# Optimization experiments

Measured on AMD Instinct MI355X. Metric: run time of the kernel, lower is better.

Reference implementation:

```python
import jax, jax.numpy as jnp
import numpy as np

N_EMBD = 1024
N_HEAD = 16
B, T = 4, 2048


def setup_inputs() -> dict:
    key = jax.random.key(0)
    k1, k2, k3, k4, k5 = jax.random.split(key, 5)
    s = 0.02
    return {
        "x": jax.random.normal(k1, (B, T, N_EMBD), dtype=jnp.float32),
        "w_attn": jax.random.normal(k2, (N_EMBD, 3 * N_EMBD), dtype=jnp.float32) * s,
        "b_attn": jnp.zeros((3 * N_EMBD,), dtype=jnp.float32),
        "w_proj": jax.random.normal(k3, (N_EMBD, N_EMBD), dtype=jnp.float32) * s,
        "b_proj": jnp.zeros((N_EMBD,), dtype=jnp.float32),
    }


def reference(x, w_attn, b_attn, w_proj, b_proj):
    Bb, Tt, C = x.shape
    hd = C // N_HEAD  # head dim
    qkv = x @ w_attn + b_attn                      # [B,T,3C]
    q, k, v = jnp.split(qkv, 3, axis=-1)
    # [B,T,C] -> [B,H,T,hd]
    def heads(t):
        return t.reshape(Bb, Tt, N_HEAD, hd).transpose(0, 2, 1, 3)
    q, k, v = heads(q), heads(k), heads(v)
    scale = 1.0 / np.sqrt(hd).astype(np.float32)
    attn = jnp.einsum("bhqd,bhkd->bhqk", q, k) * scale  # [B,H,T,T]
    causal = jnp.tril(jnp.ones((Tt, Tt), dtype=bool))
    attn = jnp.where(causal, attn, -jnp.inf)
    attn = jax.nn.softmax(attn, axis=-1)
    y = jnp.einsum("bhqk,bhkd->bhqd", attn, v)          # [B,H,T,hd]
    y = y.transpose(0, 2, 1, 3).reshape(Bb, Tt, C)
    return y @ w_proj + b_proj
```

## Files before the change

### kernel.cpp

```cpp
#include <hip/hip_runtime.h>
#include <cmath>


typedef short short8 __attribute__((ext_vector_type(8)));
typedef short short4v __attribute__((ext_vector_type(4)));
typedef float f32x4 __attribute__((ext_vector_type(4)));

__device__ __forceinline__ short f2bf(float f) {
  unsigned u = __builtin_bit_cast(unsigned, f);
  u = (u + 0x7fffu + ((u >> 16) & 1u)) >> 16;
  return (short)u;
}

__device__ __forceinline__ float exp2_fast(float x) {
  float r;
  asm("v_exp_f32 %0, %1" : "=v"(r) : "v"(x));
  return r;
}

__device__ __forceinline__ void gld_lds16(const void* g, void* l) {
  __builtin_amdgcn_global_load_lds(
      (__attribute__((address_space(1))) void*)g,
      (__attribute__((address_space(3))) void*)l,
      16, 0, 0);
}

__device__ __forceinline__ void barx() {
  asm volatile("s_barrier" ::: "memory");
}

template <int IMM>
__device__ __forceinline__ short8 dsr(int addr) {
  short8 d;
  asm volatile("ds_read_b128 %0, %1 offset:%2"
               : "=v"(d) : "v"(addr), "n"(IMM));
  return d;
}

#define WAITL()                                       \
  asm volatile("s_waitcnt lgkmcnt(0)" ::: "memory");  \
  __builtin_amdgcn_sched_barrier(0);

__global__ void cast_bf16_kernel(const float* __restrict__ in,
                                 short* __restrict__ out, int n4) {
  int i = blockIdx.x * blockDim.x + threadIdx.x;
  if (i < n4) {
    const float4 v = ((const float4*)in)[i];
    short4v o;
    o.x = f2bf(v.x); o.y = f2bf(v.y); o.z = f2bf(v.z); o.w = f2bf(v.w);
    ((short4v*)out)[i] = o;
  }
}

__global__ void transpose_cast_kernel(const float* __restrict__ in,
                                      short* __restrict__ out, int R, int C) {
  __shared__ float tile[32][33];
  int c0 = blockIdx.x * 32, r0 = blockIdx.y * 32;
  int tx = threadIdx.x & 31, tg = threadIdx.x >> 5;
#pragma unroll
  for (int i = 0; i < 4; ++i) {
    int r = tg * 4 + i;
    tile[r][tx] = in[(size_t)(r0 + r) * C + c0 + tx];
  }
  __syncthreads();
#pragma unroll
  for (int i = 0; i < 4; ++i) {
    int c = tg * 4 + i;
    out[(size_t)(c0 + c) * R + r0 + tx] = f2bf(tile[tx][c]);
  }
}


__global__ __launch_bounds__(512, 2) void qkv_gemm_kernel(
    const short* __restrict__ A, const short* __restrict__ Bt,
    const float* __restrict__ bias,
    short* __restrict__ oq, short* __restrict__ ok, short* __restrict__ ovt,
    int M, int N, int K) {
  extern __shared__ short lds[];
  const int NT = K >> 6;
  const int lane = threadIdx.x & 63, wave = threadIdx.x >> 6;
  const int quad = lane >> 4, l16 = lane & 15;
  const int wm2 = wave >> 2, wn4 = wave & 3;

  const int nbn = N >> 8;
  const int swz = (blockIdx.x & 7) * ((int)gridDim.x >> 3) + (blockIdx.x >> 3);
  const int m0 = (swz / nbn) * 256, n0 = (swz % nbn) * 256;

  const int r8 = lane >> 3;
  const int sw8 = ((lane & 7) ^ r8) * 8;
  const short* Ab0 = A + (size_t)(m0 + wave * 8 + r8) * K + sw8;
  const short* Bb0 = Bt + (size_t)(n0 + wave * 8 + r8) * K + sw8;
  short* ldsw = lds + wave * 512;

  auto stage = [&](int t, int mat, int rA, int rB) {
    const short* g = (mat ? Bb0 : Ab0) + t * 64;
    short* d = ldsw + (t & 1) * 32768 + mat * 16384;
    gld_lds16(g + (size_t)rA * K, d + rA * 64);
    gld_lds16(g + (size_t)rB * K, d + rB * 64);
  };

  const int swz0 = ((0 + quad) ^ (l16 & 7)) * 16;
  const int swz1 = ((4 + quad) ^ (l16 & 7)) * 16;
  const int baseA0 = wm2 * 16384 + l16 * 128 + swz0;
  const int baseA1 = wm2 * 16384 + l16 * 128 + swz1;
  const int baseB0 = 32768 + wn4 * 8192 + l16 * 128 + swz0;
  const int baseB1 = 32768 + wn4 * 8192 + l16 * 128 + swz1;

  f32x4 acc[8][4] = {};

  stage(0, 1, 0, 64);
  stage(0, 1, 128, 192);
  stage(0, 0, 0, 128);
  stage(0, 0, 64, 192);
  asm volatile("s_waitcnt vmcnt(0)" ::: "memory");
  barx();

#pragma unroll 1
  for (int t = 0; t < NT; ++t) {
    const int vb = (t & 1) << 16;
    const int aA0 = baseA0 + vb, aA1 = baseA1 + vb;
    const int aB0 = baseB0 + vb, aB1 = baseB1 + vb;
    short8 a[8], b[4];

    b[0] = dsr<0>(aB0);     b[1] = dsr<2048>(aB0);
    b[2] = dsr<4096>(aB0);  b[3] = dsr<6144>(aB0);
    a[0] = dsr<0>(aA0);     a[1] = dsr<2048>(aA0);
    a[2] = dsr<4096>(aA0);  a[3] = dsr<6144>(aA0);
    a[4] = dsr<8192>(aA0);  a[5] = dsr<10240>(aA0);
    a[6] = dsr<12288>(aA0); a[7] = dsr<14336>(aA0);
    if (t + 1 < NT) {
      stage(t + 1, 1, 0, 64);
      stage(t + 1, 1, 128, 192);
      stage(t + 1, 0, 0, 128);
      stage(t + 1, 0, 64, 192);
    }
    WAITL()
    __builtin_amdgcn_s_setprio(1);
#pragma unroll
    for (int i_ = 0; i_ < 8; ++i_)
#pragma unroll
      for (int n_ = 0; n_ < 4; ++n_)
        acc[i_][n_] = __builtin_amdgcn_mfma_f32_16x16x32_bf16(
            a[i_], b[n_], acc[i_][n_], 0, 0, 0);
    __builtin_amdgcn_s_setprio(0);

    b[0] = dsr<0>(aB1);     b[1] = dsr<2048>(aB1);
    b[2] = dsr<4096>(aB1);  b[3] = dsr<6144>(aB1);
    a[0] = dsr<0>(aA1);     a[1] = dsr<2048>(aA1);
    a[2] = dsr<4096>(aA1);  a[3] = dsr<6144>(aA1);
    a[4] = dsr<8192>(aA1);  a[5] = dsr<10240>(aA1);
    a[6] = dsr<12288>(aA1); a[7] = dsr<14336>(aA1);
    WAITL()
    __builtin_amdgcn_s_setprio(1);
#pragma unroll
    for (int i_ = 0; i_ < 8; ++i_)
#pragma unroll
      for (int n_ = 0; n_ < 4; ++n_)
        acc[i_][n_] = __builtin_amdgcn_mfma_f32_16x16x32_bf16(
            a[i_], b[n_], acc[i_][n_], 0, 0, 0);
    __builtin_amdgcn_s_setprio(0);

    if (t + 1 < NT)
      asm volatile("s_waitcnt vmcnt(0)" ::: "memory");
    barx();
  }

  const int sec = n0 >> 10;
  const int h0 = (n0 & 1023) >> 6;
  const float scale = (sec == 0) ? 0.18033688f : 1.0f;
  float bv[4];
#pragma unroll
  for (int n_ = 0; n_ < 4; ++n_) bv[n_] = bias[n0 + wn4 * 64 + n_ * 16 + l16];
  const int b_ = m0 >> 11, t0 = m0 & 2047;

  if (sec < 2) {
    short* dst = (sec == 0) ? oq : ok;
#pragma unroll 1
    for (int p = 0; p < 2; ++p) {
      if (wm2 == p) {
#pragma unroll
        for (int mt = 0; mt < 8; ++mt)
#pragma unroll
          for (int n_ = 0; n_ < 4; ++n_) {
            const int col = wn4 * 64 + n_ * 16 + l16;
#pragma unroll
            for (int r = 0; r < 4; ++r)
              lds[(mt * 16 + quad * 4 + r) * 264 + col] =
                  f2bf((acc[mt][n_][r] + bv[n_]) * scale);
          }
      }
      __syncthreads();
      const int hl = wave & 3, rg = wave >> 2;
      const short* sp = &lds[(rg * 64 + r8) * 264 + hl * 64 + (lane & 7) * 8];
      short* gp = dst +
          ((size_t)(b_ * 16 + h0 + hl) * 2048 + t0 + p * 128 + rg * 64 + r8) * 64 +
          (lane & 7) * 8;
#pragma unroll
      for (int i = 0; i < 8; ++i)
        *(short8*)(gp + (size_t)i * 512) = *(const short8*)(sp + i * 8 * 264);
      __syncthreads();
    }
  } else {
#pragma unroll 1
    for (int p = 0; p < 2; ++p) {
      if (wm2 == p) {
#pragma unroll
        for (int mt = 0; mt < 8; ++mt)
#pragma unroll
          for (int n_ = 0; n_ < 4; ++n_) {
            const int col = wn4 * 64 + n_ * 16 + l16;
#pragma unroll
            for (int r = 0; r < 4; ++r)
              lds[col * 136 + mt * 16 + quad * 4 + r] =
                  f2bf(acc[mt][n_][r] + bv[n_]);
          }
      }
      __syncthreads();
      const int cw = wave * 32 + (lane >> 4);
#pragma unroll
      for (int i = 0; i < 8; ++i) {
        const int c = cw + i * 4;
        const int bh = b_ * 16 + h0 + (c >> 6), d = c & 63;
        *(short8*)(ovt + ((size_t)bh * 64 + d) * 2048 + t0 + p * 128 +
                   (lane & 15) * 8) =
            *(const short8*)&lds[c * 136 + (lane & 15) * 8];
      }
      __syncthreads();
    }
  }
}

template <int MODE>
__global__ __launch_bounds__(256) void gemm_bt_kernel(
    const short* __restrict__ A, const short* __restrict__ Bt,
    const float* __restrict__ bias, float* __restrict__ outf,
    short* __restrict__ oq, short* __restrict__ ok, short* __restrict__ ovt,
    int M, int N, int K) {
  __shared__ short slds[16384];
  short* As = slds;
  short* Bs = slds + 8192;
  const int m0 = blockIdx.y * 128, n0 = blockIdx.x * 128;
  const int lane = threadIdx.x & 63, wave = threadIdx.x >> 6;
  const int quad = lane >> 4, l16 = lane & 15;
  const int wm = (wave >> 1) * 64, wn = (wave & 1) * 64;

  const int row_off = lane >> 3;
  const int segsw = ((lane & 7) ^ row_off) * 8;
  const short* Ag = A + (size_t)(m0 + wave * 32 + row_off) * K + segsw;
  const short* Bg = Bt + (size_t)(n0 + wave * 32 + row_off) * K + segsw;

  f32x4 acc[4][4] = {};

  for (int k0 = 0; k0 < K; k0 += 64) {
#pragma unroll
    for (int g = 0; g < 4; ++g) {
      gld_lds16(Ag + (size_t)(g * 8) * K + k0, &As[(wave * 32 + g * 8) * 64]);
      gld_lds16(Bg + (size_t)(g * 8) * K + k0, &Bs[(wave * 32 + g * 8) * 64]);
    }
    __syncthreads();
#pragma unroll
    for (int kh = 0; kh < 2; ++kh) {
      short8 a[4], b[4];
#pragma unroll
      for (int t = 0; t < 4; ++t) {
        const int R = wm + t * 16 + l16;
        a[t] = *(const short8*)&As[R * 64 + (((kh * 4 + quad) ^ (R & 7)) * 8)];
      }
#pragma unroll
      for (int t = 0; t < 4; ++t) {
        const int R = wn + t * 16 + l16;
        b[t] = *(const short8*)&Bs[R * 64 + (((kh * 4 + quad) ^ (R & 7)) * 8)];
      }
#pragma unroll
      for (int mt = 0; mt < 4; ++mt)
#pragma unroll
        for (int nt = 0; nt < 4; ++nt)
          acc[mt][nt] = __builtin_amdgcn_mfma_f32_16x16x32_bf16(
              a[mt], b[nt], acc[mt][nt], 0, 0, 0);
    }
    __syncthreads();
  }

  float bv[4];
#pragma unroll
  for (int nt = 0; nt < 4; ++nt) bv[nt] = bias[n0 + wn + nt * 16 + l16];

  if (MODE == 1) {
#pragma unroll
    for (int mt = 0; mt < 4; ++mt)
#pragma unroll
      for (int nt = 0; nt < 4; ++nt) {
        const int n = n0 + wn + nt * 16 + l16;
#pragma unroll
        for (int r = 0; r < 4; ++r) {
          const int m = m0 + wm + mt * 16 + quad * 4 + r;
          outf[(size_t)m * N + n] = acc[mt][nt][r] + bv[nt];
        }
      }
  }
}

__global__ __launch_bounds__(256, 6) void attn_kernel(
    const short* __restrict__ q, const short* __restrict__ k,
    const short* __restrict__ vt, short* __restrict__ y) {
  __shared__ short Ks[64 * 64];
  __shared__ short Vs[64 * 64];
  __shared__ short Ps[4][16 * 72];
  const int lane = threadIdx.x & 63, wave = threadIdx.x >> 6;
  const int quad = lane >> 4, l16 = lane & 15;
  const int g = blockIdx.x;
  const int bh = g & 63;
  const int j = 31 - (g >> 6);
  const int b_ = bh >> 4, h = bh & 15;
  const int q0 = j * 64 + wave * 16;

  const short* qbh = q + (size_t)bh * 2048 * 64;
  const short* kbh = k + (size_t)bh * 2048 * 64;
  const short* vbh = vt + (size_t)bh * 64 * 2048;
  short* Pw = Ps[wave];

  const short8 qf0 = *(const short8*)&qbh[(q0 + l16) * 64 + quad * 8];
  const short8 qf1 = *(const short8*)&qbh[(q0 + l16) * 64 + 32 + quad * 8];

  short8 ones;
#pragma unroll
  for (int i = 0; i < 8; ++i) ones[i] = (short)0x3F80;

  f32x4 O[4] = {};
  f32x4 lacc = {};

  const int srow = lane >> 3;
  const int scol = ((lane & 7) ^ srow) * 8;
  const int r0s = wave * 16;

#pragma unroll 1
  for (int c = 0; c <= j; ++c) {
    const int kt0 = c * 64;
    gld_lds16(kbh + (size_t)(kt0 + r0s + srow) * 64 + scol, &Ks[r0s * 64]);
    gld_lds16(kbh + (size_t)(kt0 + r0s + 8 + srow) * 64 + scol, &Ks[(r0s + 8) * 64]);
    gld_lds16(vbh + (size_t)(r0s + srow) * 2048 + kt0 + scol, &Vs[r0s * 64]);
    gld_lds16(vbh + (size_t)(r0s + 8 + srow) * 2048 + kt0 + scol, &Vs[(r0s + 8) * 64]);
    __syncthreads();

    const int sw = l16 & 7;
    f32x4 sc4[4];
#pragma unroll
    for (int cf = 0; cf < 4; ++cf) {
      const int row = cf * 16 + l16;
      const short8 kfa = *(const short8*)&Ks[row * 64 + ((quad ^ sw) * 8)];
      const short8 kfb = *(const short8*)&Ks[row * 64 + (((quad + 4) ^ sw) * 8)];
      f32x4 z = {};
      z = __builtin_amdgcn_mfma_f32_16x16x32_bf16(qf0, kfa, z, 0, 0, 0);
      z = __builtin_amdgcn_mfma_f32_16x16x32_bf16(qf1, kfb, z, 0, 0, 0);
      sc4[cf] = z;
    }

    if (c == j) {
#pragma unroll
      for (int cf = 0; cf < 4; ++cf) {
        const int col = kt0 + cf * 16 + l16;
#pragma unroll
        for (int r = 0; r < 4; ++r) {
          const int rowg = q0 + quad * 4 + r;
          float e = exp2_fast(sc4[cf][r]);
          e = (col > rowg) ? 0.f : e;
          Pw[(quad * 4 + r) * 72 + cf * 16 + l16] = f2bf(e);
        }
      }
    } else {
#pragma unroll
      for (int cf = 0; cf < 4; ++cf)
#pragma unroll
        for (int r = 0; r < 4; ++r)
          Pw[(quad * 4 + r) * 72 + cf * 16 + l16] = f2bf(exp2_fast(sc4[cf][r]));
    }
    asm volatile("s_waitcnt lgkmcnt(0)" ::: "memory");
    const short8 pf0 = *(const short8*)&Pw[l16 * 72 + quad * 8];
    const short8 pf1 = *(const short8*)&Pw[l16 * 72 + 32 + quad * 8];

    lacc = __builtin_amdgcn_mfma_f32_16x16x32_bf16(pf0, ones, lacc, 0, 0, 0);
    lacc = __builtin_amdgcn_mfma_f32_16x16x32_bf16(pf1, ones, lacc, 0, 0, 0);

#pragma unroll
    for (int dt = 0; dt < 4; ++dt) {
      const int d = dt * 16 + l16;
      const short8 vf0 = *(const short8*)&Vs[d * 64 + ((quad ^ sw) * 8)];
      const short8 vf1 = *(const short8*)&Vs[d * 64 + (((quad + 4) ^ sw) * 8)];
      O[dt] = __builtin_amdgcn_mfma_f32_16x16x32_bf16(pf0, vf0, O[dt], 0, 0, 0);
      O[dt] = __builtin_amdgcn_mfma_f32_16x16x32_bf16(pf1, vf1, O[dt], 0, 0, 0);
    }
    __syncthreads();
  }

  float inv[4];
#pragma unroll
  for (int r = 0; r < 4; ++r) inv[r] = 1.0f / lacc[r];
#pragma unroll
  for (int dt = 0; dt < 4; ++dt) {
    const int d = dt * 16 + l16;
#pragma unroll
    for (int r = 0; r < 4; ++r) {
      const int t_ = q0 + quad * 4 + r;
      y[((size_t)b_ * 2048 + t_) * 1024 + h * 64 + d] = f2bf(O[dt][r] * inv[r]);
    }
  }
}

extern "C" void kernel_launch(void* const* d_in, const int* in_sizes, int n_in,
                              void* d_out, int out_size, void* d_ws, size_t ws_size,
                              hipStream_t stream) {
  const float* x      = (const float*)d_in[0];
  const float* w_attn = (const float*)d_in[1];
  const float* b_attn = (const float*)d_in[2];
  const float* w_proj = (const float*)d_in[3];
  const float* b_proj = (const float*)d_in[4];
  float* out = (float*)d_out;

  short* xb  = (short*)d_ws;
  short* wTa = xb + (size_t)8192 * 1024;
  short* wTp = wTa + (size_t)3072 * 1024;
  short* qb  = wTp + (size_t)1024 * 1024;
  short* kb  = qb + (size_t)64 * 2048 * 64;
  short* vtb = kb + (size_t)64 * 2048 * 64;
  short* yb  = vtb + (size_t)64 * 2048 * 64;

  static int lds_attr_done = 0;
  if (!lds_attr_done) {
    (void)hipFuncSetAttribute(reinterpret_cast<const void*>(qkv_gemm_kernel),
                              hipFuncAttributeMaxDynamicSharedMemorySize,
                              131072);
    lds_attr_done = 1;
  }

  cast_bf16_kernel<<<8192, 256, 0, stream>>>(x, xb, 8192 * 1024 / 4);
  transpose_cast_kernel<<<dim3(96, 32), 256, 0, stream>>>(w_attn, wTa, 1024, 3072);
  transpose_cast_kernel<<<dim3(32, 32), 256, 0, stream>>>(w_proj, wTp, 1024, 1024);

  qkv_gemm_kernel<<<384, 512, 131072, stream>>>(
      xb, wTa, b_attn, qb, kb, vtb, 8192, 3072, 1024);

  attn_kernel<<<2048, 256, 0, stream>>>(qb, kb, vtb, yb);

  gemm_bt_kernel<1><<<dim3(8, 64), 256, 0, stream>>>(
      yb, wTp, b_proj, out, nullptr, nullptr, nullptr, 8192, 1024, 1024);
}
```

Baseline: 244.7 us.

## Shrink QKV GEMM tile to 128x256 and issue both LDS read halves early

The QKV projection GEMM block tile is cut from 256x256 to 128x256. That doubles the grid to 768 blocks, cuts LDS to 96 KB, and halves the accumulator registers, so more blocks can run at once and the 256 CUs are better filled. Both k-halves of the LDS fragments are now read up front, with a partial lgkmcnt wait, so the second half's reads overlap the first half's MFMAs. The epilogue drops its two-pass loop because the whole tile fits in LDS at once. In exchange, operand reuse per block is lower and global/L2 traffic for the B matrix rises.

```diff
diff --git a/kernel.cpp b/kernel.cpp
--- a/kernel.cpp
+++ b/kernel.cpp
@@ -37,8 +37,8 @@
   return d;
 }
 
-#define WAITL()                                       \
-  asm volatile("s_waitcnt lgkmcnt(0)" ::: "memory");  \
+#define WAITLN(n)                                          \
+  asm volatile("s_waitcnt lgkmcnt(" #n ")" ::: "memory");  \
   __builtin_amdgcn_sched_barrier(0);
 
 __global__ void cast_bf16_kernel(const float* __restrict__ in,
@@ -84,7 +84,7 @@
 
   const int nbn = N >> 8;
   const int swz = (blockIdx.x & 7) * ((int)gridDim.x >> 3) + (blockIdx.x >> 3);
-  const int m0 = (swz / nbn) * 256, n0 = (swz % nbn) * 256;
+  const int m0 = (swz / nbn) * 128, n0 = (swz % nbn) * 256;
 
   const int r8 = lane >> 3;
   const int sw8 = ((lane & 7) ^ r8) * 8;
@@ -94,70 +94,65 @@
 
   auto stage = [&](int t, int mat, int rA, int rB) {
     const short* g = (mat ? Bb0 : Ab0) + t * 64;
-    short* d = ldsw + (t & 1) * 32768 + mat * 16384;
+    short* d = ldsw + (t & 1) * 24576 + mat * 8192;
     gld_lds16(g + (size_t)rA * K, d + rA * 64);
     gld_lds16(g + (size_t)rB * K, d + rB * 64);
   };
 
   const int swz0 = ((0 + quad) ^ (l16 & 7)) * 16;
   const int swz1 = ((4 + quad) ^ (l16 & 7)) * 16;
-  const int baseA0 = wm2 * 16384 + l16 * 128 + swz0;
-  const int baseA1 = wm2 * 16384 + l16 * 128 + swz1;
-  const int baseB0 = 32768 + wn4 * 8192 + l16 * 128 + swz0;
-  const int baseB1 = 32768 + wn4 * 8192 + l16 * 128 + swz1;
-
-  f32x4 acc[8][4] = {};
+  const int baseA0 = wm2 * 8192 + l16 * 128 + swz0;
+  const int baseA1 = wm2 * 8192 + l16 * 128 + swz1;
+  const int baseB0 = 16384 + wn4 * 8192 + l16 * 128 + swz0;
+  const int baseB1 = 16384 + wn4 * 8192 + l16 * 128 + swz1;
+
+  f32x4 acc[4][4] = {};
 
   stage(0, 1, 0, 64);
   stage(0, 1, 128, 192);
-  stage(0, 0, 0, 128);
-  stage(0, 0, 64, 192);
+  stage(0, 0, 0, 64);
   asm volatile("s_waitcnt vmcnt(0)" ::: "memory");
   barx();
 
 #pragma unroll 1
   for (int t = 0; t < NT; ++t) {
-    const int vb = (t & 1) << 16;
+    const int vb = (t & 1) * 49152;
     const int aA0 = baseA0 + vb, aA1 = baseA1 + vb;
     const int aB0 = baseB0 + vb, aB1 = baseB1 + vb;
-    short8 a[8], b[4];
-
-    b[0] = dsr<0>(aB0);     b[1] = dsr<2048>(aB0);
-    b[2] = dsr<4096>(aB0);  b[3] = dsr<6144>(aB0);
-    a[0] = dsr<0>(aA0);     a[1] = dsr<2048>(aA0);
-    a[2] = dsr<4096>(aA0);  a[3] = dsr<6144>(aA0);
-    a[4] = dsr<8192>(aA0);  a[5] = dsr<10240>(aA0);
-    a[6] = dsr<12288>(aA0); a[7] = dsr<14336>(aA0);
+    short8 a0[4], b0[4], a1[4], b1[4];
+
+    b0[0] = dsr<0>(aB0);     b0[1] = dsr<2048>(aB0);
+    b0[2] = dsr<4096>(aB0);  b0[3] = dsr<6144>(aB0);
+    a0[0] = dsr<0>(aA0);     a0[1] = dsr<2048>(aA0);
+    a0[2] = dsr<4096>(aA0);  a0[3] = dsr<6144>(aA0);
     if (t + 1 < NT) {
       stage(t + 1, 1, 0, 64);
       stage(t + 1, 1, 128, 192);
-      stage(t + 1, 0, 0, 128);
-      stage(t + 1, 0, 64, 192);
-    }
-    WAITL()
+      stage(t + 1, 0, 0, 64);
+    }
+    b1[0] = dsr<0>(aB1);     b1[1] = dsr<2048>(aB1);
+    b1[2] = dsr<4096>(aB1);  b1[3] = dsr<6144>(aB1);
+    a1[0] = dsr<0>(aA1);     a1[1] = dsr<2048>(aA1);
+    a1[2] = dsr<4096>(aA1);  a1[3] = dsr<6144>(aA1);
+
+    WAITLN(8)
     __builtin_amdgcn_s_setprio(1);
 #pragma unroll
-    for (int i_ = 0; i_ < 8; ++i_)
+    for (int i_ = 0; i_ < 4; ++i_)
 #pragma unroll
       for (int n_ = 0; n_ < 4; ++n_)
         acc[i_][n_] = __builtin_amdgcn_mfma_f32_16x16x32_bf16(
-            a[i_], b[n_], acc[i_][n_], 0, 0, 0);
+            a0[i_], b0[n_], acc[i_][n_], 0, 0, 0);
     __builtin_amdgcn_s_setprio(0);
 
-    b[0] = dsr<0>(aB1);     b[1] = dsr<2048>(aB1);
-    b[2] = dsr<4096>(aB1);  b[3] = dsr<6144>(aB1);
-    a[0] = dsr<0>(aA1);     a[1] = dsr<2048>(aA1);
-    a[2] = dsr<4096>(aA1);  a[3] = dsr<6144>(aA1);
-    a[4] = dsr<8192>(aA1);  a[5] = dsr<10240>(aA1);
-    a[6] = dsr<12288>(aA1); a[7] = dsr<14336>(aA1);
-    WAITL()
+    WAITLN(0)
     __builtin_amdgcn_s_setprio(1);
 #pragma unroll
-    for (int i_ = 0; i_ < 8; ++i_)
+    for (int i_ = 0; i_ < 4; ++i_)
 #pragma unroll
       for (int n_ = 0; n_ < 4; ++n_)
         acc[i_][n_] = __builtin_amdgcn_mfma_f32_16x16x32_bf16(
-            a[i_], b[n_], acc[i_][n_], 0, 0, 0);
+            a1[i_], b1[n_], acc[i_][n_], 0, 0, 0);
     __builtin_amdgcn_s_setprio(0);
 
     if (t + 1 < NT)
@@ -173,59 +168,47 @@
   for (int n_ = 0; n_ < 4; ++n_) bv[n_] = bias[n0 + wn4 * 64 + n_ * 16 + l16];
   const int b_ = m0 >> 11, t0 = m0 & 2047;
 
+  __syncthreads();
   if (sec < 2) {
     short* dst = (sec == 0) ? oq : ok;
-#pragma unroll 1
-    for (int p = 0; p < 2; ++p) {
-      if (wm2 == p) {
-#pragma unroll
-        for (int mt = 0; mt < 8; ++mt)
-#pragma unroll
-          for (int n_ = 0; n_ < 4; ++n_) {
-            const int col = wn4 * 64 + n_ * 16 + l16;
-#pragma unroll
-            for (int r = 0; r < 4; ++r)
-              lds[(mt * 16 + quad * 4 + r) * 264 + col] =
-                  f2bf((acc[mt][n_][r] + bv[n_]) * scale);
-          }
-      }
-      __syncthreads();
-      const int hl = wave & 3, rg = wave >> 2;
-      const short* sp = &lds[(rg * 64 + r8) * 264 + hl * 64 + (lane & 7) * 8];
-      short* gp = dst +
-          ((size_t)(b_ * 16 + h0 + hl) * 2048 + t0 + p * 128 + rg * 64 + r8) * 64 +
-          (lane & 7) * 8;
-#pragma unroll
-      for (int i = 0; i < 8; ++i)
-        *(short8*)(gp + (size_t)i * 512) = *(const short8*)(sp + i * 8 * 264);
-      __syncthreads();
-    }
+#pragma unroll
+    for (int mt = 0; mt < 4; ++mt)
+#pragma unroll
+      for (int n_ = 0; n_ < 4; ++n_) {
+        const int col = wn4 * 64 + n_ * 16 + l16;
+#pragma unroll
+        for (int r = 0; r < 4; ++r)
+          lds[(wm2 * 64 + mt * 16 + quad * 4 + r) * 264 + col] =
+              f2bf((acc[mt][n_][r] + bv[n_]) * scale);
+      }
+    __syncthreads();
+    const int hl = wave & 3, rg = wave >> 2;
+    const short* sp = &lds[(rg * 64 + r8) * 264 + hl * 64 + (lane & 7) * 8];
+    short* gp = dst +
+        ((size_t)(b_ * 16 + h0 + hl) * 2048 + t0 + rg * 64 + r8) * 64 +
+        (lane & 7) * 8;
+#pragma unroll
+    for (int i = 0; i < 8; ++i)
+      *(short8*)(gp + (size_t)i * 512) = *(const short8*)(sp + i * 8 * 264);
   } else {
-#pragma unroll 1
-    for (int p = 0; p < 2; ++p) {
-      if (wm2 == p) {
-#pragma unroll
-        for (int mt = 0; mt < 8; ++mt)
-#pragma unroll
-          for (int n_ = 0; n_ < 4; ++n_) {
-            const int col = wn4 * 64 + n_ * 16 + l16;
-#pragma unroll
-            for (int r = 0; r < 4; ++r)
-              lds[col * 136 + mt * 16 + quad * 4 + r] =
-                  f2bf(acc[mt][n_][r] + bv[n_]);
-          }
-      }
-      __syncthreads();
-      const int cw = wave * 32 + (lane >> 4);
-#pragma unroll
-      for (int i = 0; i < 8; ++i) {
-        const int c = cw + i * 4;
-        const int bh = b_ * 16 + h0 + (c >> 6), d = c & 63;
-        *(short8*)(ovt + ((size_t)bh * 64 + d) * 2048 + t0 + p * 128 +
-                   (lane & 15) * 8) =
-            *(const short8*)&lds[c * 136 + (lane & 15) * 8];
-      }
-      __syncthreads();
+#pragma unroll
+    for (int mt = 0; mt < 4; ++mt)
+#pragma unroll
+      for (int n_ = 0; n_ < 4; ++n_) {
+        const int col = wn4 * 64 + n_ * 16 + l16;
+#pragma unroll
+        for (int r = 0; r < 4; ++r)
+          lds[col * 136 + wm2 * 64 + mt * 16 + quad * 4 + r] =
+              f2bf(acc[mt][n_][r] + bv[n_]);
+      }
+    __syncthreads();
+    const int cw = wave * 32 + (lane >> 4);
+#pragma unroll
+    for (int i = 0; i < 8; ++i) {
+      const int c = cw + i * 4;
+      const int bh = b_ * 16 + h0 + (c >> 6), d = c & 63;
+      *(short8*)(ovt + ((size_t)bh * 64 + d) * 2048 + t0 + (lane & 15) * 8) =
+          *(const short8*)&lds[c * 136 + (lane & 15) * 8];
     }
   }
 }
@@ -428,7 +411,7 @@
   if (!lds_attr_done) {
     (void)hipFuncSetAttribute(reinterpret_cast<const void*>(qkv_gemm_kernel),
                               hipFuncAttributeMaxDynamicSharedMemorySize,
-                              131072);
+                              98304);
     lds_attr_done = 1;
   }
 
@@ -436,7 +419,7 @@
   transpose_cast_kernel<<<dim3(96, 32), 256, 0, stream>>>(w_attn, wTa, 1024, 3072);
   transpose_cast_kernel<<<dim3(32, 32), 256, 0, stream>>>(w_proj, wTp, 1024, 1024);
 
-  qkv_gemm_kernel<<<384, 512, 131072, stream>>>(
+  qkv_gemm_kernel<<<768, 512, 98304, stream>>>(
       xb, wTa, b_attn, qb, kb, vtb, 8192, 3072, 1024);
 
   attn_kernel<<<2048, 256, 0, stream>>>(qb, kb, vtb, yb);
```

Measured after the change: 242.7 us. No clear change (-0.8%).
